# Optimization experiments

Hardware: AMD Instinct MI355X
Metric: run time of the kernel (lower is better)

The kernel has to match this reference:

```python
import jax, jax.numpy as jnp
import numpy as np

N, C, H, W = 4, 64, 64, 64
K = 3


def _unfold(x, k):
    """torch F.unfold with padding k//2: [n,c,h,w] -> [n, c*k*k, h*w].
    Feature ordering matches torch: index = c*k*k + i*k + j."""
    p = k // 2
    n, c, h, w = x.shape
    xp = jnp.pad(x, ((0, 0), (0, 0), (p, p), (p, p)))
    patches = jnp.stack(
        [xp[:, :, i:i + h, j:j + w] for i in range(k) for j in range(k)], axis=2
    )  # [n, c, k*k, h, w]
    return patches.reshape(n, c * k * k, h * w)


def _mask_vec(c, k):
    # causal patch mask from __init__: zero out center-and-right of middle row and all rows below
    m = np.ones((c, k, k), np.float32)
    m[:, k // 2, k // 2:] = 0
    m[:, k // 2 + 1:, :] = 0
    return jnp.asarray(m.reshape(1, c * k * k, 1))


def setup_inputs() -> dict:
    key = jax.random.key(0)
    k1, k2 = jax.random.split(key)
    y_hat = jax.random.normal(k1, (N, C, H, W), dtype=jnp.float32)
    y_prob = jax.random.uniform(k2, (N, 1, H, W), dtype=jnp.float32)
    return {"y_hat": y_hat, "y_prob": y_prob}


def reference(y_hat, y_prob):
    k = K
    n, c, h, w = y_hat.shape
    L = h * w
    mask = _mask_vec(c, k)

    u = _unfold(y_hat, k) * mask                              # [n, c*k*k, L]
    u = u / jnp.maximum(jnp.linalg.norm(u, axis=1, keepdims=True), 1e-12)
    R = jnp.einsum('nfl,nfm->nlm', u, u)                      # [n, L, L] cosine sims

    # eval path: keep strictly-upper triangle (causal: l < m)
    row = jnp.arange(L)[:, None]
    col = jnp.arange(L)[None, :]
    R = jnp.where(col > row, R, 0.0)

    R_star = jnp.max(R, axis=1)                               # [n, L]
    arg = jnp.argmax(R, axis=1).astype(jnp.int32)             # [n, L]

    y_unf = _unfold(y_hat, k)                                 # [n, c*k*k, L]
    ref_unfold = jnp.take_along_axis(y_unf, arg[:, None, :], axis=2)

    prob_unf = y_prob.reshape(n, -1, L)                       # 1x1 unfold
    U_unf = jnp.take_along_axis(prob_unf, arg[:, None, :], axis=2)

    S = R_star.reshape(n, 1, h, w)
    U = U_unf.reshape(n, -1, h, w)

    # eval-mode position-0 overrides
    S = S.at[:, :, 0, 0].set(1e-8)
    U = U.at[:, :, 0, 0].set(1e-8)
    ref_unfold = ref_unfold.at[:, :, 0].set(0.0)
    arg = arg.at[:, 0].set(-1)

    S = jnp.clip(S, 1e-8, 1.0)
    U = jnp.clip(U, 1e-8, 1.0)
    return S, U, ref_unfold, arg
```

## Files before the change

### kernel.cpp

```cpp
#include <hip/hip_runtime.h>
#include <stdint.h>

#define Nn 4
#define Cc 64
#define LL 4096
#define KK 256
#define NB 32
#define TRI2 528
#define PAD_H 40

typedef _Float16 half8 __attribute__((ext_vector_type(8)));
typedef float f32x16 __attribute__((ext_vector_type(16)));
typedef float f4a __attribute__((ext_vector_type(4), aligned(4)));

__device__ __forceinline__ unsigned f2ord(float f) {
    unsigned u = __float_as_uint(f);
    return u ^ ((u & 0x80000000u) ? 0xFFFFFFFFu : 0x80000000u);
}
__device__ __forceinline__ float ord2f(unsigned o) {
    unsigned u = (o & 0x80000000u) ? (o ^ 0x80000000u) : ~o;
    return __uint_as_float(u);
}
__device__ __forceinline__ unsigned short h2u(_Float16 h) {
    union { _Float16 f; unsigned short u; } x; x.f = h; return x.u;
}

__global__ __launch_bounds__(256) void build_v(const float* __restrict__ yhat,
                                               unsigned short* __restrict__ VhT,
                                               unsigned short* __restrict__ VlT) {
    int gid = blockIdx.x * 256 + threadIdx.x;
    int cg = gid & 15;
    int nl = gid >> 4;
    int l = nl & (LL - 1);
    int n = nl >> 12;
    int y = l >> 6, x = l & 63;
    const float* src = yhat + (size_t)n * (Cc * LL);

    float vals[16];
    float sumsq = 0.f;
#pragma unroll
    for (int ci = 0; ci < 4; ++ci) {
        const float* p = src + (cg * 4 + ci) * LL;
        float t0 = (y > 0 && x > 0)  ? p[l - 65] : 0.f;
        float t1 = (y > 0)           ? p[l - 64] : 0.f;
        float t2 = (y > 0 && x < 63) ? p[l - 63] : 0.f;
        float t3 = (x > 0)           ? p[l - 1]  : 0.f;
        vals[ci * 4 + 0] = t0; vals[ci * 4 + 1] = t1;
        vals[ci * 4 + 2] = t2; vals[ci * 4 + 3] = t3;
        sumsq += t0 * t0 + t1 * t1 + t2 * t2 + t3 * t3;
    }
    sumsq += __shfl_xor(sumsq, 1, 64);
    sumsq += __shfl_xor(sumsq, 2, 64);
    sumsq += __shfl_xor(sumsq, 4, 64);
    sumsq += __shfl_xor(sumsq, 8, 64);
    float inv = 1.f / fmaxf(sqrtf(sumsq), 1e-12f);

    unsigned short* dh = VhT + (size_t)nl * KK + cg * 16;
    unsigned short* dl = VlT + (size_t)nl * KK + cg * 16;
#pragma unroll
    for (int ci = 0; ci < 4; ++ci) {
        ushort4 hv, lv;
        unsigned short* ph = &hv.x;
        unsigned short* pl = &lv.x;
#pragma unroll
        for (int tp = 0; tp < 4; ++tp) {
            float v = vals[ci * 4 + tp] * inv;
            _Float16 h = (fabsf(v) < 6.1035e-5f) ? (_Float16)0 : (_Float16)v;
            _Float16 lo = (_Float16)((v - (float)h) * 2048.0f);
            ph[tp] = h2u(h * (_Float16)2048.0f);
            pl[tp] = h2u(lo);
        }
        *(ushort4*)(dh + ci * 4) = hv;
        *(ushort4*)(dl + ci * 4) = lv;
    }
}

__global__ __launch_bounds__(256) void simmax(const unsigned short* __restrict__ Vh,
                                              const unsigned short* __restrict__ Vl,
                                              unsigned long long* __restrict__ best) {
    __shared__ __align__(16) unsigned short Ah[128 * PAD_H];
    __shared__ __align__(16) unsigned short Al[128 * PAD_H];
    __shared__ __align__(16) unsigned short Bh[128 * PAD_H];
    __shared__ __align__(16) unsigned short Bl[128 * PAD_H];

    int bx = blockIdx.x;
    int xcd = bx & 7, idx = bx >> 3;
    int n = xcd >> 1;
    int t = (xcd & 1) * 264 + idx;
    int j = (int)((sqrtf(8.f * (float)t + 1.f) - 1.f) * 0.5f);
    while ((j + 1) * (j + 2) / 2 <= t) ++j;
    while (j * (j + 1) / 2 > t) --j;
    int i = t - j * (j + 1) / 2;
    int l0 = i * 128, m0 = j * 128;

    const unsigned short* VhB = Vh + (size_t)n * (LL * KK);
    const unsigned short* VlB = Vl + (size_t)n * (LL * KK);

    int tid = threadIdx.x;
    int w = tid >> 6, lane = tid & 63;
    int r5 = lane & 31, h5 = lane >> 5;
    int rw = (w & 1) * 64;
    int cw = (w >> 1) * 64;
    bool skip = (i == j) && (rw == 64) && (cw == 0);

    f32x16 acc[2][2];
#pragma unroll
    for (int r = 0; r < 2; ++r)
#pragma unroll
        for (int c = 0; c < 2; ++c) acc[r][c] = (f32x16)0.f;

    int srow = tid >> 2;
    int sh = (tid & 3) * 8;

    for (int k0 = 0; k0 < KK; k0 += 32) {
        const size_t ra = (size_t)(l0 + srow) * KK + k0 + sh;
        const size_t rb = (size_t)(l0 + 64 + srow) * KK + k0 + sh;
        const size_t rc = (size_t)(m0 + srow) * KK + k0 + sh;
        const size_t rd = (size_t)(m0 + 64 + srow) * KK + k0 + sh;
        uint4 ah0 = *(const uint4*)(VhB + ra);
        uint4 ah1 = *(const uint4*)(VhB + rb);
        uint4 al0 = *(const uint4*)(VlB + ra);
        uint4 al1 = *(const uint4*)(VlB + rb);
        uint4 bh0 = *(const uint4*)(VhB + rc);
        uint4 bh1 = *(const uint4*)(VhB + rd);
        uint4 bl0 = *(const uint4*)(VlB + rc);
        uint4 bl1 = *(const uint4*)(VlB + rd);
        __syncthreads();
        *(uint4*)&Ah[srow * PAD_H + sh]        = ah0;
        *(uint4*)&Ah[(64 + srow) * PAD_H + sh] = ah1;
        *(uint4*)&Al[srow * PAD_H + sh]        = al0;
        *(uint4*)&Al[(64 + srow) * PAD_H + sh] = al1;
        *(uint4*)&Bh[srow * PAD_H + sh]        = bh0;
        *(uint4*)&Bh[(64 + srow) * PAD_H + sh] = bh1;
        *(uint4*)&Bl[srow * PAD_H + sh]        = bl0;
        *(uint4*)&Bl[(64 + srow) * PAD_H + sh] = bl1;
        __syncthreads();
        if (!skip) {
            half8 fah[2][2], fal[2][2], fbh[2][2], fbl[2][2];
#pragma unroll
            for (int r = 0; r < 2; ++r)
#pragma unroll
                for (int kc = 0; kc < 2; ++kc) {
                    int ao = (rw + r * 32 + r5) * PAD_H + kc * 16 + h5 * 8;
                    int bo = (cw + r * 32 + r5) * PAD_H + kc * 16 + h5 * 8;
                    fah[r][kc] = *(half8*)&Ah[ao];
                    fal[r][kc] = *(half8*)&Al[ao];
                    fbh[r][kc] = *(half8*)&Bh[bo];
                    fbl[r][kc] = *(half8*)&Bl[bo];
                }
#pragma unroll
            for (int kc = 0; kc < 2; ++kc)
#pragma unroll
                for (int r = 0; r < 2; ++r)
#pragma unroll
                    for (int c = 0; c < 2; ++c)
                        acc[r][c] = __builtin_amdgcn_mfma_f32_32x32x16_f16(fal[r][kc], fbh[c][kc], acc[r][c], 0, 0, 0);
#pragma unroll
            for (int kc = 0; kc < 2; ++kc)
#pragma unroll
                for (int r = 0; r < 2; ++r)
#pragma unroll
                    for (int c = 0; c < 2; ++c)
                        acc[r][c] = __builtin_amdgcn_mfma_f32_32x32x16_f16(fah[r][kc], fbl[c][kc], acc[r][c], 0, 0, 0);
#pragma unroll
            for (int kc = 0; kc < 2; ++kc)
#pragma unroll
                for (int r = 0; r < 2; ++r)
#pragma unroll
                    for (int c = 0; c < 2; ++c)
                        acc[r][c] = __builtin_amdgcn_mfma_f32_32x32x16_f16(fah[r][kc], fbh[c][kc], acc[r][c], 0, 0, 0);
        }
    }

    if (skip) return;
    unsigned long long* bb = best + (size_t)n * LL;
    const float s = 1.f / 4194304.f;
#pragma unroll
    for (int c = 0; c < 2; ++c) {
        int m = m0 + cw + c * 32 + r5;
        unsigned long long key = 0ull;
#pragma unroll
        for (int r = 0; r < 2; ++r)
#pragma unroll
            for (int g = 0; g < 16; ++g) {
                int l = l0 + rw + r * 32 + (g & 3) + 8 * (g >> 2) + 4 * h5;
                if (l < m) {
                    float v = acc[r][c][g] * s;
                    unsigned long long k2 =
                        ((unsigned long long)f2ord(v) << 32) |
                        (unsigned long long)(0xFFFFFFFFu - (unsigned)l);
                    key = (k2 > key) ? k2 : key;
                }
            }
        unsigned long long o = __shfl_xor(key, 32, 64);
        key = (o > key) ? o : key;
        if (h5 == 0 && key != 0ull) atomicMax(bb + m, key);
    }
}

__global__ __launch_bounds__(256) void writeout(const float* __restrict__ yhat,
                                                const float* __restrict__ yprob,
                                                const unsigned long long* __restrict__ best,
                                                float* __restrict__ out) {
    int bx = blockIdx.x;
    int n = bx >> 8;
    int mb = (bx >> 2) & 63;
    int fc = bx & 3;
    int tid = threadIdx.x;
    int mm = tid & 63;
    int fs = tid >> 6;
    int m = mb * 64 + mm;

    unsigned long long key = best[(size_t)n * LL + m];
    unsigned l = 0xFFFFFFFFu - (unsigned)(key & 0xFFFFFFFFull);
    float val = ord2f((unsigned)(key >> 32));
    bool zero = (m == 0);
    if (zero) l = 0;
    int ly = (int)(l >> 6), lx = (int)(l & 63);

    float* Sout = out;
    float* Uout = out + 16384;
    float* Rout = out + 32768;
    float* Aout = out + 9469952;

    if (fc == 0 && fs == 0) {
        float S = zero ? 1e-8f : fminf(fmaxf(val, 1e-8f), 1.0f);
        float U = zero ? 1e-8f : fminf(fmaxf(yprob[(size_t)n * LL + l], 1e-8f), 1.0f);
        Sout[(size_t)n * LL + m] = S;
        Uout[(size_t)n * LL + m] = U;
        Aout[(size_t)n * LL + m] = zero ? -1.0f : (float)l;
    }

    const float* src = yhat + (size_t)n * (Cc * LL);
    float* dst = Rout + (size_t)n * (576 * LL) + m;
    bool fast = (!zero) && (lx >= 1) && (lx <= 61);
#pragma unroll
    for (int cc = 0; cc < 4; ++cc) {
        int c = fc * 16 + fs * 4 + cc;
        const float* plane = src + (size_t)c * LL;
#pragma unroll
        for (int r3 = 0; r3 < 3; ++r3) {
            int yy = ly + r3 - 1;
            bool rowok = (!zero) && (yy >= 0) && (yy < 64);
            float t0 = 0.f, t1 = 0.f, t2 = 0.f;
            if (rowok) {
                if (fast) {
                    f4a v = *(const f4a*)(plane + yy * 64 + lx - 1);
                    t0 = v.x; t1 = v.y; t2 = v.z;
                } else {
                    if (lx > 0)  t0 = plane[yy * 64 + lx - 1];
                    t1 = plane[yy * 64 + lx];
                    if (lx < 63) t2 = plane[yy * 64 + lx + 1];
                }
            }
            size_t f = (size_t)(c * 9 + r3 * 3) * LL;
            __builtin_nontemporal_store(t0, dst + f);
            __builtin_nontemporal_store(t1, dst + f + LL);
            __builtin_nontemporal_store(t2, dst + f + 2 * (size_t)LL);
        }
    }
}

extern "C" void kernel_launch(void* const* d_in, const int* in_sizes, int n_in,
                              void* d_out, int out_size, void* d_ws, size_t ws_size,
                              hipStream_t stream) {
    const float* yhat  = (const float*)d_in[0];
    const float* yprob = (const float*)d_in[1];
    float* out = (float*)d_out;

    unsigned short* VhT = (unsigned short*)d_ws;
    unsigned short* VlT = (unsigned short*)((char*)d_ws + 8388608);
    unsigned long long* best =
        (unsigned long long*)((char*)d_ws + 16777216);

    hipMemsetAsync(best, 0, (size_t)Nn * LL * sizeof(unsigned long long), stream);
    build_v<<<1024, 256, 0, stream>>>(yhat, VhT, VlT);
    simmax<<<Nn * TRI2, 256, 0, stream>>>(VhT, VlT, best);
    writeout<<<Nn * 64 * 4, 256, 0, stream>>>(yhat, yprob, best, out);
}
```

Baseline: 162.8 us.

## Widen simmax tiles to 128x256, use direct global-to-LDS loads, fuse memset

The similarity-max kernel now computes 128x256 tiles, so each wave does 64x128 with 8 accumulators. Operands are staged with global_load_lds into a single XOR-swizzled shared buffer, with launch bounds set for 2 blocks per CU. build_v is restructured to stage two image rows in LDS and also zeroes the best array, which removes the separate memset launch. This is meant to cut global traffic per FLOP and launch overhead, at the cost of more register pressure and a coarser triangular tiling that wastes some upper-triangle work.

```diff
diff --git a/kernel.cpp b/kernel.cpp
--- a/kernel.cpp
+++ b/kernel.cpp
@@ -5,9 +5,6 @@
 #define Cc 64
 #define LL 4096
 #define KK 256
-#define NB 32
-#define TRI2 528
-#define PAD_H 40
 
 typedef _Float16 half8 __attribute__((ext_vector_type(8)));
 typedef float f32x16 __attribute__((ext_vector_type(16)));
@@ -27,44 +24,69 @@
 
 __global__ __launch_bounds__(256) void build_v(const float* __restrict__ yhat,
                                                unsigned short* __restrict__ VhT,
-                                               unsigned short* __restrict__ VlT) {
-    int gid = blockIdx.x * 256 + threadIdx.x;
-    int cg = gid & 15;
-    int nl = gid >> 4;
-    int l = nl & (LL - 1);
-    int n = nl >> 12;
-    int y = l >> 6, x = l & 63;
+                                               unsigned short* __restrict__ VlT,
+                                               unsigned long long* __restrict__ best) {
+    __shared__ float P[4096];
+    __shared__ float Cr[4096];
+    int b = blockIdx.x;
+    int n = b >> 6, y = b & 63;
+    int tid = threadIdx.x;
+    if (tid < 64) best[(size_t)n * LL + y * 64 + tid] = 0ull;
+
     const float* src = yhat + (size_t)n * (Cc * LL);
-
-    float vals[16];
+#pragma unroll
+    for (int k = 0; k < 8; ++k) {
+        int f4i = tid + 256 * k;
+        int plane = f4i >> 10;
+        int rem = f4i & 1023;
+        int ch = rem >> 4, xq = rem & 15;
+        if (plane == 0) {
+            float4 v = make_float4(0.f, 0.f, 0.f, 0.f);
+            if (y > 0) v = *(const float4*)(src + (size_t)ch * LL + (y - 1) * 64 + xq * 4);
+            *(float4*)&P[ch * 64 + xq * 4] = v;
+        } else {
+            float4 v = *(const float4*)(src + (size_t)ch * LL + y * 64 + xq * 4);
+            *(float4*)&Cr[ch * 64 + xq * 4] = v;
+        }
+    }
+    __syncthreads();
+
+    int cq = tid & 3, x = tid >> 2;
     float sumsq = 0.f;
 #pragma unroll
-    for (int ci = 0; ci < 4; ++ci) {
-        const float* p = src + (cg * 4 + ci) * LL;
-        float t0 = (y > 0 && x > 0)  ? p[l - 65] : 0.f;
-        float t1 = (y > 0)           ? p[l - 64] : 0.f;
-        float t2 = (y > 0 && x < 63) ? p[l - 63] : 0.f;
-        float t3 = (x > 0)           ? p[l - 1]  : 0.f;
-        vals[ci * 4 + 0] = t0; vals[ci * 4 + 1] = t1;
-        vals[ci * 4 + 2] = t2; vals[ci * 4 + 3] = t3;
+    for (int ci = 0; ci < 16; ++ci) {
+        int ch = cq * 16 + ci;
+        const float* pp = &P[ch * 64];
+        const float* pc = &Cr[ch * 64];
+        float t0 = (x > 0)  ? pp[x - 1] : 0.f;
+        float t1 = pp[x];
+        float t2 = (x < 63) ? pp[x + 1] : 0.f;
+        float t3 = (x > 0)  ? pc[x - 1] : 0.f;
         sumsq += t0 * t0 + t1 * t1 + t2 * t2 + t3 * t3;
     }
     sumsq += __shfl_xor(sumsq, 1, 64);
     sumsq += __shfl_xor(sumsq, 2, 64);
-    sumsq += __shfl_xor(sumsq, 4, 64);
-    sumsq += __shfl_xor(sumsq, 8, 64);
     float inv = 1.f / fmaxf(sqrtf(sumsq), 1e-12f);
 
-    unsigned short* dh = VhT + (size_t)nl * KK + cg * 16;
-    unsigned short* dl = VlT + (size_t)nl * KK + cg * 16;
-#pragma unroll
-    for (int ci = 0; ci < 4; ++ci) {
+    size_t nl = (size_t)n * LL + y * 64 + x;
+    unsigned short* dh = VhT + nl * KK + cq * 64;
+    unsigned short* dl = VlT + nl * KK + cq * 64;
+#pragma unroll
+    for (int ci = 0; ci < 16; ++ci) {
+        int ch = cq * 16 + ci;
+        const float* pp = &P[ch * 64];
+        const float* pc = &Cr[ch * 64];
+        float t[4];
+        t[0] = (x > 0)  ? pp[x - 1] : 0.f;
+        t[1] = pp[x];
+        t[2] = (x < 63) ? pp[x + 1] : 0.f;
+        t[3] = (x > 0)  ? pc[x - 1] : 0.f;
         ushort4 hv, lv;
         unsigned short* ph = &hv.x;
         unsigned short* pl = &lv.x;
 #pragma unroll
         for (int tp = 0; tp < 4; ++tp) {
-            float v = vals[ci * 4 + tp] * inv;
+            float v = t[tp] * inv;
             _Float16 h = (fabsf(v) < 6.1035e-5f) ? (_Float16)0 : (_Float16)v;
             _Float16 lo = (_Float16)((v - (float)h) * 2048.0f);
             ph[tp] = h2u(h * (_Float16)2048.0f);
@@ -75,23 +97,20 @@
     }
 }
 
-__global__ __launch_bounds__(256) void simmax(const unsigned short* __restrict__ Vh,
-                                              const unsigned short* __restrict__ Vl,
-                                              unsigned long long* __restrict__ best) {
-    __shared__ __align__(16) unsigned short Ah[128 * PAD_H];
-    __shared__ __align__(16) unsigned short Al[128 * PAD_H];
-    __shared__ __align__(16) unsigned short Bh[128 * PAD_H];
-    __shared__ __align__(16) unsigned short Bl[128 * PAD_H];
+__global__ __launch_bounds__(256, 2) void simmax(const unsigned short* __restrict__ Vh,
+                                                 const unsigned short* __restrict__ Vl,
+                                                 unsigned long long* __restrict__ best) {
+    __shared__ __align__(16) unsigned short S[24576];
 
     int bx = blockIdx.x;
     int xcd = bx & 7, idx = bx >> 3;
     int n = xcd >> 1;
-    int t = (xcd & 1) * 264 + idx;
-    int j = (int)((sqrtf(8.f * (float)t + 1.f) - 1.f) * 0.5f);
-    while ((j + 1) * (j + 2) / 2 <= t) ++j;
-    while (j * (j + 1) / 2 > t) --j;
-    int i = t - j * (j + 1) / 2;
-    int l0 = i * 128, m0 = j * 128;
+    int t = (xcd & 1) * 136 + idx;
+    int J = (int)((sqrtf(4.f * (float)t + 1.f) - 1.f) * 0.5f);
+    while ((J + 1) * (J + 2) <= t) ++J;
+    while (J * (J + 1) > t) --J;
+    int i = t - J * (J + 1);
+    int l0 = i * 128, m0 = J * 256;
 
     const unsigned short* VhB = Vh + (size_t)n * (LL * KK);
     const unsigned short* VlB = Vl + (size_t)n * (LL * KK);
@@ -100,92 +119,91 @@
     int w = tid >> 6, lane = tid & 63;
     int r5 = lane & 31, h5 = lane >> 5;
     int rw = (w & 1) * 64;
-    int cw = (w >> 1) * 64;
-    bool skip = (i == j) && (rw == 64) && (cw == 0);
-
-    f32x16 acc[2][2];
+    int cw = (w >> 1) * 128;
+    bool skip = (l0 + rw) > (m0 + cw + 127);
+
+    f32x16 acc[2][4];
 #pragma unroll
     for (int r = 0; r < 2; ++r)
 #pragma unroll
-        for (int c = 0; c < 2; ++c) acc[r][c] = (f32x16)0.f;
-
-    int srow = tid >> 2;
-    int sh = (tid & 3) * 8;
+        for (int c = 0; c < 4; ++c) acc[r][c] = (f32x16)0.f;
+
+    int rl = lane >> 2, cl = lane & 3;
+    int arow0 = rw + r5, arow1 = rw + 32 + r5;
+    int sA0 = (arow0 >> 1) & 3, sA1 = (arow1 >> 1) & 3;
+    int brow[4], sB[4];
+#pragma unroll
+    for (int ct = 0; ct < 4; ++ct) {
+        brow[ct] = cw + ct * 32 + r5;
+        sB[ct] = (brow[ct] >> 1) & 3;
+    }
 
     for (int k0 = 0; k0 < KK; k0 += 32) {
-        const size_t ra = (size_t)(l0 + srow) * KK + k0 + sh;
-        const size_t rb = (size_t)(l0 + 64 + srow) * KK + k0 + sh;
-        const size_t rc = (size_t)(m0 + srow) * KK + k0 + sh;
-        const size_t rd = (size_t)(m0 + 64 + srow) * KK + k0 + sh;
-        uint4 ah0 = *(const uint4*)(VhB + ra);
-        uint4 ah1 = *(const uint4*)(VhB + rb);
-        uint4 al0 = *(const uint4*)(VlB + ra);
-        uint4 al1 = *(const uint4*)(VlB + rb);
-        uint4 bh0 = *(const uint4*)(VhB + rc);
-        uint4 bh1 = *(const uint4*)(VhB + rd);
-        uint4 bl0 = *(const uint4*)(VlB + rc);
-        uint4 bl1 = *(const uint4*)(VlB + rd);
-        __syncthreads();
-        *(uint4*)&Ah[srow * PAD_H + sh]        = ah0;
-        *(uint4*)&Ah[(64 + srow) * PAD_H + sh] = ah1;
-        *(uint4*)&Al[srow * PAD_H + sh]        = al0;
-        *(uint4*)&Al[(64 + srow) * PAD_H + sh] = al1;
-        *(uint4*)&Bh[srow * PAD_H + sh]        = bh0;
-        *(uint4*)&Bh[(64 + srow) * PAD_H + sh] = bh1;
-        *(uint4*)&Bl[srow * PAD_H + sh]        = bl0;
-        *(uint4*)&Bl[(64 + srow) * PAD_H + sh] = bl1;
+#pragma unroll
+        for (int qq = 0; qq < 12; ++qq) {
+            int q = w * 12 + qq;
+            int buf = (q < 8) ? 0 : (q < 16) ? 1 : (q < 32) ? 2 : 3;
+            int rg = q - ((buf == 0) ? 0 : (buf == 1) ? 8 : (buf == 2) ? 16 : 32);
+            const unsigned short* srcb = (buf & 1) ? VlB : VhB;
+            int tile0 = (buf < 2) ? l0 : m0;
+            int row_local = rg * 16 + rl;
+            int cg = cl ^ ((row_local >> 1) & 3);
+            const unsigned short* gp = srcb + (size_t)(tile0 + row_local) * KK + k0 + cg * 8;
+            int hb = ((buf == 0) ? 0 : (buf == 1) ? 4096 : (buf == 2) ? 8192 : 16384) + rg * 512;
+            __builtin_amdgcn_global_load_lds(
+                (const __attribute__((address_space(1))) unsigned int*)(uintptr_t)gp,
+                (__attribute__((address_space(3))) unsigned int*)(uintptr_t)(&S[hb]),
+                16, 0, 0);
+        }
         __syncthreads();
         if (!skip) {
-            half8 fah[2][2], fal[2][2], fbh[2][2], fbl[2][2];
-#pragma unroll
-            for (int r = 0; r < 2; ++r)
-#pragma unroll
-                for (int kc = 0; kc < 2; ++kc) {
-                    int ao = (rw + r * 32 + r5) * PAD_H + kc * 16 + h5 * 8;
-                    int bo = (cw + r * 32 + r5) * PAD_H + kc * 16 + h5 * 8;
-                    fah[r][kc] = *(half8*)&Ah[ao];
-                    fal[r][kc] = *(half8*)&Al[ao];
-                    fbh[r][kc] = *(half8*)&Bh[bo];
-                    fbl[r][kc] = *(half8*)&Bl[bo];
-                }
-#pragma unroll
-            for (int kc = 0; kc < 2; ++kc)
-#pragma unroll
-                for (int r = 0; r < 2; ++r)
-#pragma unroll
-                    for (int c = 0; c < 2; ++c)
-                        acc[r][c] = __builtin_amdgcn_mfma_f32_32x32x16_f16(fal[r][kc], fbh[c][kc], acc[r][c], 0, 0, 0);
-#pragma unroll
-            for (int kc = 0; kc < 2; ++kc)
-#pragma unroll
-                for (int r = 0; r < 2; ++r)
-#pragma unroll
-                    for (int c = 0; c < 2; ++c)
-                        acc[r][c] = __builtin_amdgcn_mfma_f32_32x32x16_f16(fah[r][kc], fbl[c][kc], acc[r][c], 0, 0, 0);
-#pragma unroll
-            for (int kc = 0; kc < 2; ++kc)
-#pragma unroll
-                for (int r = 0; r < 2; ++r)
-#pragma unroll
-                    for (int c = 0; c < 2; ++c)
-                        acc[r][c] = __builtin_amdgcn_mfma_f32_32x32x16_f16(fah[r][kc], fbh[c][kc], acc[r][c], 0, 0, 0);
-        }
+#pragma unroll
+            for (int kc = 0; kc < 2; ++kc) {
+                int c0 = kc * 2 + h5;
+                half8 fah0 = *(half8*)&S[arow0 * 32 + ((c0 ^ sA0) * 8)];
+                half8 fah1 = *(half8*)&S[arow1 * 32 + ((c0 ^ sA1) * 8)];
+                half8 fal0 = *(half8*)&S[4096 + arow0 * 32 + ((c0 ^ sA0) * 8)];
+                half8 fal1 = *(half8*)&S[4096 + arow1 * 32 + ((c0 ^ sA1) * 8)];
+                half8 fbh[4], fbl[4];
+#pragma unroll
+                for (int ct = 0; ct < 4; ++ct) {
+                    fbh[ct] = *(half8*)&S[8192 + brow[ct] * 32 + ((c0 ^ sB[ct]) * 8)];
+                    fbl[ct] = *(half8*)&S[16384 + brow[ct] * 32 + ((c0 ^ sB[ct]) * 8)];
+                }
+#pragma unroll
+                for (int ct = 0; ct < 4; ++ct) {
+                    acc[0][ct] = __builtin_amdgcn_mfma_f32_32x32x16_f16(fal0, fbh[ct], acc[0][ct], 0, 0, 0);
+                    acc[1][ct] = __builtin_amdgcn_mfma_f32_32x32x16_f16(fal1, fbh[ct], acc[1][ct], 0, 0, 0);
+                }
+#pragma unroll
+                for (int ct = 0; ct < 4; ++ct) {
+                    acc[0][ct] = __builtin_amdgcn_mfma_f32_32x32x16_f16(fah0, fbl[ct], acc[0][ct], 0, 0, 0);
+                    acc[1][ct] = __builtin_amdgcn_mfma_f32_32x32x16_f16(fah1, fbl[ct], acc[1][ct], 0, 0, 0);
+                }
+#pragma unroll
+                for (int ct = 0; ct < 4; ++ct) {
+                    acc[0][ct] = __builtin_amdgcn_mfma_f32_32x32x16_f16(fah0, fbh[ct], acc[0][ct], 0, 0, 0);
+                    acc[1][ct] = __builtin_amdgcn_mfma_f32_32x32x16_f16(fah1, fbh[ct], acc[1][ct], 0, 0, 0);
+                }
+            }
+        }
+        __syncthreads();
     }
 
     if (skip) return;
     unsigned long long* bb = best + (size_t)n * LL;
     const float s = 1.f / 4194304.f;
 #pragma unroll
-    for (int c = 0; c < 2; ++c) {
-        int m = m0 + cw + c * 32 + r5;
+    for (int ct = 0; ct < 4; ++ct) {
+        int m = m0 + cw + ct * 32 + r5;
         unsigned long long key = 0ull;
 #pragma unroll
-        for (int r = 0; r < 2; ++r)
+        for (int rt = 0; rt < 2; ++rt)
 #pragma unroll
             for (int g = 0; g < 16; ++g) {
-                int l = l0 + rw + r * 32 + (g & 3) + 8 * (g >> 2) + 4 * h5;
+                int l = l0 + rw + rt * 32 + (g & 3) + 8 * (g >> 2) + 4 * h5;
                 if (l < m) {
-                    float v = acc[r][c][g] * s;
+                    float v = acc[rt][ct][g] * s;
                     unsigned long long k2 =
                         ((unsigned long long)f2ord(v) << 32) |
                         (unsigned long long)(0xFFFFFFFFu - (unsigned)l);
@@ -273,8 +291,7 @@
     unsigned long long* best =
         (unsigned long long*)((char*)d_ws + 16777216);
 
-    hipMemsetAsync(best, 0, (size_t)Nn * LL * sizeof(unsigned long long), stream);
-    build_v<<<1024, 256, 0, stream>>>(yhat, VhT, VlT);
-    simmax<<<Nn * TRI2, 256, 0, stream>>>(VhT, VlT, best);
+    build_v<<<256, 256, 0, stream>>>(yhat, VhT, VlT, best);
+    simmax<<<Nn * 272, 256, 0, stream>>>(VhT, VlT, best);
     writeout<<<Nn * 64 * 4, 256, 0, stream>>>(yhat, yprob, best, out);
 }
```

Measured after the change: 170.4 us. +4.7%, slower.
